# Optimization experiments

Measured on AMD Instinct MI355X. Metric: run time of the kernel, lower is better.

The kernel has to match this reference:

```python
import jax, jax.numpy as jnp
import numpy as np

HEADS = 8
HEIGHT = 64
WIDTH = 64
LN_EPS = 1e-5


def setup_inputs() -> dict:
    key = jax.random.key(0)
    k1, k2, k3, k4 = jax.random.split(key, 4)
    B, N, D = 8, 4096, 512
    return {
        "x1": jax.random.normal(k1, (B, N, D), jnp.float32),
        "x2": jax.random.normal(k2, (B, N, D), jnp.float32),
        "conv_w": jax.random.normal(k3, (2 * D, D), jnp.float32) * 0.02,
        "conv_b": jax.random.normal(k4, (2 * D,), jnp.float32) * 0.02,
        "ln_w": jnp.ones((2 * D,), jnp.float32),
        "ln_b": jnp.zeros((2 * D,), jnp.float32),
    }


def reference(x1, x2, conv_w, conv_b, ln_w, ln_b):
    B, N, D = x1.shape
    Dk = x2.shape[-1]
    hk = Dk // HEADS  # key channels per head
    hv = D // HEADS   # value channels per head
    # [B, H, hk, N] and [B, H, hv, N] (channel-first like torch transpose(1,2))
    kq = jnp.transpose(x2, (0, 2, 1)).reshape(B, HEADS, hk, N)
    v = jnp.transpose(x1, (0, 2, 1)).reshape(B, HEADS, hv, N)
    key = jax.nn.softmax(kq, axis=-1)   # softmax over tokens N
    query = jax.nn.softmax(kq, axis=2)  # softmax over head channels
    # linear attention: context [B,H,hk,hv], attended [B,H,hv,N]
    context = jnp.einsum("bhkn,bhvn->bhkv", key, v)
    attended = jnp.einsum("bhkv,bhkn->bhvn", context, query)
    agg = attended.reshape(B, D, N)  # concat heads along channel dim
    # 1x1 conv D -> 2D, then permute to [B, N, 2D]
    y = jnp.einsum("ed,bdn->bne", conv_w, agg) + conv_b
    # LayerNorm over last dim
    mu = jnp.mean(y, axis=-1, keepdims=True)
    var = jnp.mean(jnp.square(y - mu), axis=-1, keepdims=True)
    return (y - mu) * jax.lax.rsqrt(var + LN_EPS) * ln_w + ln_b
```

## Files before the change

kernel.cpp:

```cpp
#include <hip/hip_runtime.h>
#include <hip/hip_bf16.h>


typedef short short8 __attribute__((ext_vector_type(8)));
typedef float f32x4 __attribute__((ext_vector_type(4)));
typedef unsigned int uint;
typedef unsigned short ushort;

__device__ __forceinline__ ushort f2bf(float x) {
  union { float f; uint u; } v; v.f = x;
  uint r = v.u + 0x7FFFu + ((v.u >> 16) & 1u);
  return (ushort)(r >> 16);
}

__device__ __forceinline__ void gld_lds16(const void* g, void* l) {
  __builtin_amdgcn_global_load_lds(
      (const __attribute__((address_space(1))) unsigned int*)g,
      (__attribute__((address_space(3))) unsigned int*)l, 16, 0, 0);
}

__global__ __launch_bounds__(512) void k1_colstats(const float* __restrict__ x2,
                                                   float* __restrict__ pmax,
                                                   float* __restrict__ psum) {
  int blk = blockIdx.x;
  int b = blk >> 5, ch = blk & 31;
  int d = threadIdx.x;
  const float* base = x2 + ((size_t)(b * 4096 + ch * 128) * 512) + d;
  float m = -1e30f, s = 0.f;
  for (int nn = 0; nn < 128; ++nn) {
    float v = base[(size_t)nn * 512];
    if (v > m) { s = s * __expf(m - v) + 1.f; m = v; }
    else       { s += __expf(v - m); }
  }
  int o = (b * 32 + ch) * 512 + d;
  pmax[o] = m; psum[o] = s;
}

__global__ __launch_bounds__(256) void k1b_combine(const float* __restrict__ pmax,
                                                   const float* __restrict__ psum,
                                                   float* __restrict__ M,
                                                   float* __restrict__ Z) {
  int gid = blockIdx.x * 256 + threadIdx.x;
  int b = gid >> 9, d = gid & 511;
  float m = -1e30f;
  for (int ch = 0; ch < 32; ++ch) m = fmaxf(m, pmax[(b * 32 + ch) * 512 + d]);
  float z = 0.f;
  for (int ch = 0; ch < 32; ++ch)
    z += psum[(b * 32 + ch) * 512 + d] * __expf(pmax[(b * 32 + ch) * 512 + d] - m);
  M[gid] = m; Z[gid] = z;
}

__global__ __launch_bounds__(256) void kzero(float* __restrict__ p) {
  p[blockIdx.x * 256 + threadIdx.x] = 0.f;
}

__global__ __launch_bounds__(256) void kwb(const float* __restrict__ w,
                                           ushort* __restrict__ wb) {
  int i = blockIdx.x * 256 + threadIdx.x;
  wb[i] = f2bf(w[i]);
}

__global__ __launch_bounds__(256) void k2_context(const float* __restrict__ x1,
                                                  const float* __restrict__ x2,
                                                  const float* __restrict__ M,
                                                  const float* __restrict__ Z,
                                                  float* __restrict__ ctx) {
  int blk = blockIdx.x;
  int s = blk & 15, h = (blk >> 4) & 7, b = blk >> 7;
  __shared__ alignas(16) ushort Esm[64 * 72];
  __shared__ alignas(16) ushort Vsm[64 * 72];
  int tid = threadIdx.x;
  int l = tid & 63, w = tid >> 6;
  int lr = l & 15, lg = l >> 4;
  f32x4 acc[4] = {};

  for (int sub = 0; sub < 4; ++sub) {
    int n0 = s * 256 + sub * 64;
    __syncthreads();
    #pragma unroll
    for (int i = 0; i < 16; ++i) {
      int idx = tid + i * 256;
      int kk = idx & 63, nn = idx >> 6;
      size_t g = ((size_t)(b * 4096 + n0 + nn)) * 512 + h * 64 + kk;
      float e = __expf(x2[g] - M[b * 512 + h * 64 + kk]);
      Esm[kk * 72 + nn] = f2bf(e);
      Vsm[kk * 72 + nn] = f2bf(x1[g]);
    }
    __syncthreads();
    #pragma unroll
    for (int k2 = 0; k2 < 2; ++k2) {
      short8 a = *(const short8*)&Esm[(w * 16 + lr) * 72 + k2 * 32 + lg * 8];
      #pragma unroll
      for (int n = 0; n < 4; ++n) {
        short8 bb = *(const short8*)&Vsm[(n * 16 + lr) * 72 + k2 * 32 + lg * 8];
        acc[n] = __builtin_amdgcn_mfma_f32_16x16x32_bf16(a, bb, acc[n], 0, 0, 0);
      }
    }
  }
  #pragma unroll
  for (int n = 0; n < 4; ++n) {
    #pragma unroll
    for (int j = 0; j < 4; ++j) {
      int k = w * 16 + lg * 4 + j;
      int c = n * 16 + lr;
      float val = acc[n][j] / Z[b * 512 + h * 64 + k];
      atomicAdd(&ctx[((size_t)(b * 8 + h)) * 4096 + k * 64 + c], val);
    }
  }
}

__global__ __launch_bounds__(512) void k3_agg(const float* __restrict__ x2,
                                              const float* __restrict__ ctx,
                                              ushort* __restrict__ agg) {
  int blk = blockIdx.x;
  int b = blk >> 5, s2 = blk & 31;
  int tid = threadIdx.x;
  int w = tid >> 6;
  int l = tid & 63;
  float creg[64];
  #pragma unroll
  for (int k = 0; k < 64; ++k)
    creg[k] = ctx[((size_t)(b * 8 + w)) * 4096 + k * 64 + l];

  for (int tt = 0; tt < 128; ++tt) {
    int t = s2 * 128 + tt;
    float val = x2[((size_t)(b * 4096 + t)) * 512 + w * 64 + l];
    float m = val;
    #pragma unroll
    for (int o = 32; o > 0; o >>= 1) m = fmaxf(m, __shfl_xor(m, o));
    float e = __expf(val - m);
    float z = e;
    #pragma unroll
    for (int o = 32; o > 0; o >>= 1) z += __shfl_xor(z, o);
    float acc = 0.f;
    #pragma unroll
    for (int k = 0; k < 64; ++k) {
      float ek = __int_as_float(__builtin_amdgcn_readlane(__float_as_int(e), k));
      acc += ek * creg[k];
    }
    acc /= z;
    agg[((size_t)(b * 4096 + t)) * 512 + w * 64 + l] = f2bf(acc);
  }
}

__global__ __launch_bounds__(256) void k4_gemm(const ushort* __restrict__ agg,
                                               const ushort* __restrict__ wb,
                                               const float* __restrict__ conv_b,
                                               float* __restrict__ out) {
  int bm = blockIdx.x >> 3;
  int bn = blockIdx.x & 7;
  __shared__ alignas(16) ushort Asm[128 * 32];
  __shared__ alignas(16) ushort Bsm[128 * 32];
  int tid = threadIdx.x;
  int l = tid & 63, w = tid >> 6;
  int lr = l & 15, lg = l >> 4;
  int wr = (w >> 1) * 64, wc = (w & 1) * 64;
  f32x4 acc[4][4] = {};
  int rowA = bm * 128, rowB = bn * 128;
  int srow = tid >> 2;
  int skel = (tid & 3) * 8;

  for (int k0 = 0; k0 < 512; k0 += 32) {
    __syncthreads();
    #pragma unroll
    for (int c = 0; c < 2; ++c) {
      const ushort* ga = agg + (size_t)(rowA + c * 64 + srow) * 512 + k0 + skel;
      const ushort* gb = wb  + (size_t)(rowB + c * 64 + srow) * 512 + k0 + skel;
      gld_lds16(ga, (char*)Asm + c * 4096 + w * 1024);
      gld_lds16(gb, (char*)Bsm + c * 4096 + w * 1024);
    }
    __syncthreads();
    short8 a[4], bf[4];
    #pragma unroll
    for (int m = 0; m < 4; ++m)
      a[m] = *(const short8*)&Asm[(wr + m * 16 + lr) * 32 + lg * 8];
    #pragma unroll
    for (int n = 0; n < 4; ++n)
      bf[n] = *(const short8*)&Bsm[(wc + n * 16 + lr) * 32 + lg * 8];
    #pragma unroll
    for (int m = 0; m < 4; ++m)
      #pragma unroll
      for (int n = 0; n < 4; ++n)
        acc[m][n] = __builtin_amdgcn_mfma_f32_16x16x32_bf16(a[m], bf[n], acc[m][n], 0, 0, 0);
  }

  #pragma unroll
  for (int n = 0; n < 4; ++n) {
    int col = rowB + wc + n * 16 + lr;
    float bv = conv_b[col];
    #pragma unroll
    for (int m = 0; m < 4; ++m) {
      int row0 = rowA + wr + m * 16 + lg * 4;
      #pragma unroll
      for (int j = 0; j < 4; ++j)
        out[(size_t)(row0 + j) * 1024 + col] = acc[m][n][j] + bv;
    }
  }
}

__global__ __launch_bounds__(256) void k5_ln(float* __restrict__ out,
                                             const float* __restrict__ lnw,
                                             const float* __restrict__ lnb) {
  int t = blockIdx.x;
  int tid = threadIdx.x;
  float4 v = ((const float4*)(out + (size_t)t * 1024))[tid];
  float s  = v.x + v.y + v.z + v.w;
  float s2 = v.x * v.x + v.y * v.y + v.z * v.z + v.w * v.w;
  #pragma unroll
  for (int o = 32; o > 0; o >>= 1) { s += __shfl_xor(s, o); s2 += __shfl_xor(s2, o); }
  __shared__ float red[8];
  int w = tid >> 6, l = tid & 63;
  if (l == 0) { red[w] = s; red[4 + w] = s2; }
  __syncthreads();
  s  = red[0] + red[1] + red[2] + red[3];
  s2 = red[4] + red[5] + red[6] + red[7];
  float mean = s * (1.f / 1024.f);
  float var  = s2 * (1.f / 1024.f) - mean * mean;
  float rstd = rsqrtf(fmaxf(var, 0.f) + 1e-5f);
  float4 wv = ((const float4*)lnw)[tid];
  float4 bv = ((const float4*)lnb)[tid];
  float4 o;
  o.x = (v.x - mean) * rstd * wv.x + bv.x;
  o.y = (v.y - mean) * rstd * wv.y + bv.y;
  o.z = (v.z - mean) * rstd * wv.z + bv.z;
  o.w = (v.w - mean) * rstd * wv.w + bv.w;
  ((float4*)(out + (size_t)t * 1024))[tid] = o;
}

extern "C" void kernel_launch(void* const* d_in, const int* in_sizes, int n_in,
                              void* d_out, int out_size, void* d_ws, size_t ws_size,
                              hipStream_t stream) {
  const float* x1     = (const float*)d_in[0];
  const float* x2     = (const float*)d_in[1];
  const float* conv_w = (const float*)d_in[2];
  const float* conv_b = (const float*)d_in[3];
  const float* ln_w   = (const float*)d_in[4];
  const float* ln_b   = (const float*)d_in[5];
  float* out = (float*)d_out;

  float* ws   = (float*)d_ws;
  float* M    = ws;
  float* Z    = M + 4096;
  float* pmax = Z + 4096;
  float* psum = pmax + 131072;
  float* ctx  = psum + 131072;
  ushort* aggb = (ushort*)(ctx + 262144);
  ushort* wbb  = aggb + 16777216;

  k1_colstats<<<256, 512, 0, stream>>>(x2, pmax, psum);
  k1b_combine<<<16, 256, 0, stream>>>(pmax, psum, M, Z);
  kzero<<<1024, 256, 0, stream>>>(ctx);
  kwb<<<2048, 256, 0, stream>>>(conv_w, wbb);
  k2_context<<<1024, 256, 0, stream>>>(x1, x2, M, Z, ctx);
  k3_agg<<<256, 512, 0, stream>>>(x2, ctx, aggb);
  k4_gemm<<<2048, 256, 0, stream>>>(aggb, wbb, conv_b, out);
  k5_ln<<<32768, 256, 0, stream>>>(out, ln_w, ln_b);
}
```

Baseline: 550.7 us.

## Fold per-batch context into conv weights and feed query softmax to GEMM

The attended-value step is reassociated: the per-head context is multiplied into the 1x1 conv weight to form a per-batch weight W2[b] = W·ctx. The big GEMM then consumes the channel-softmaxed query directly. This removes the serial readlane-based aggregation kernel, which had low occupancy, and replaces it with a vectorized softmax kernel plus a small weight-folding kernel. The cost is that each batch now has its own bf16 weight matrix, which reduces weight reuse across batches in the GEMM and adds the precision risk of rounding the folded weights to bf16.

```diff
diff --git a/kernel.cpp b/kernel.cpp
--- a/kernel.cpp
+++ b/kernel.cpp
@@ -54,12 +54,6 @@
   p[blockIdx.x * 256 + threadIdx.x] = 0.f;
 }
 
-__global__ __launch_bounds__(256) void kwb(const float* __restrict__ w,
-                                           ushort* __restrict__ wb) {
-  int i = blockIdx.x * 256 + threadIdx.x;
-  wb[i] = f2bf(w[i]);
-}
-
 __global__ __launch_bounds__(256) void k2_context(const float* __restrict__ x1,
                                                   const float* __restrict__ x2,
                                                   const float* __restrict__ M,
@@ -109,46 +103,78 @@
   }
 }
 
-__global__ __launch_bounds__(512) void k3_agg(const float* __restrict__ x2,
-                                              const float* __restrict__ ctx,
-                                              ushort* __restrict__ agg) {
-  int blk = blockIdx.x;
-  int b = blk >> 5, s2 = blk & 31;
-  int tid = threadIdx.x;
-  int w = tid >> 6;
-  int l = tid & 63;
-  float creg[64];
-  #pragma unroll
-  for (int k = 0; k < 64; ++k)
-    creg[k] = ctx[((size_t)(b * 8 + w)) * 4096 + k * 64 + l];
-
-  for (int tt = 0; tt < 128; ++tt) {
-    int t = s2 * 128 + tt;
-    float val = x2[((size_t)(b * 4096 + t)) * 512 + w * 64 + l];
-    float m = val;
-    #pragma unroll
-    for (int o = 32; o > 0; o >>= 1) m = fmaxf(m, __shfl_xor(m, o));
-    float e = __expf(val - m);
-    float z = e;
-    #pragma unroll
-    for (int o = 32; o > 0; o >>= 1) z += __shfl_xor(z, o);
-    float acc = 0.f;
-    #pragma unroll
-    for (int k = 0; k < 64; ++k) {
-      float ek = __int_as_float(__builtin_amdgcn_readlane(__float_as_int(e), k));
-      acc += ek * creg[k];
-    }
-    acc /= z;
-    agg[((size_t)(b * 4096 + t)) * 512 + w * 64 + l] = f2bf(acc);
-  }
-}
-
-__global__ __launch_bounds__(256) void k4_gemm(const ushort* __restrict__ agg,
-                                               const ushort* __restrict__ wb,
+__global__ __launch_bounds__(256) void kq_softmax(const float* __restrict__ x2,
+                                                  ushort* __restrict__ Q) {
+  int tid = threadIdx.x;
+  int tok = blockIdx.x * 2 + (tid >> 7);
+  int c4 = (tid & 127) * 4;
+  float4 v = *(const float4*)(x2 + (size_t)tok * 512 + c4);
+  float m = fmaxf(fmaxf(v.x, v.y), fmaxf(v.z, v.w));
+  #pragma unroll
+  for (int o = 1; o < 16; o <<= 1) m = fmaxf(m, __shfl_xor(m, o));
+  float ex = __expf(v.x - m), ey = __expf(v.y - m);
+  float ez = __expf(v.z - m), ew = __expf(v.w - m);
+  float z = ex + ey + ez + ew;
+  #pragma unroll
+  for (int o = 1; o < 16; o <<= 1) z += __shfl_xor(z, o);
+  float rz = 1.f / z;
+  ushort4 q;
+  q.x = f2bf(ex * rz); q.y = f2bf(ey * rz);
+  q.z = f2bf(ez * rz); q.w = f2bf(ew * rz);
+  *(ushort4*)(Q + (size_t)tok * 512 + c4) = q;
+}
+
+__global__ __launch_bounds__(256) void kw2(const float* __restrict__ W,
+                                           const float* __restrict__ ctx,
+                                           ushort* __restrict__ W2) {
+  int blk = blockIdx.x;
+  int ec = blk & 7, h = (blk >> 3) & 7, b = blk >> 6;
+  __shared__ float Csm[64 * 68];
+  __shared__ float Wsm[128 * 68];
+  int tid = threadIdx.x;
+  const float* cp = ctx + ((size_t)(b * 8 + h)) * 4096;
+  #pragma unroll
+  for (int i = 0; i < 4; ++i) {
+    int idx = tid + i * 256, k = idx >> 4, cc = (idx & 15) * 4;
+    float4 cv = *(const float4*)(cp + k * 64 + cc);
+    *(float4*)(Csm + k * 68 + cc) = cv;
+  }
+  int e0 = ec * 128;
+  #pragma unroll
+  for (int i = 0; i < 8; ++i) {
+    int idx = tid + i * 256, r = idx >> 4, cc = (idx & 15) * 4;
+    float4 wv = *(const float4*)(W + (size_t)(e0 + r) * 512 + h * 64 + cc);
+    *(float4*)(Wsm + r * 68 + cc) = wv;
+  }
+  __syncthreads();
+  int r = tid >> 3;
+  int kg = (tid & 7) * 8;
+  for (int rs = 0; rs < 4; ++rs) {
+    int row = rs * 32 + r;
+    float acc[8] = {0.f, 0.f, 0.f, 0.f, 0.f, 0.f, 0.f, 0.f};
+    #pragma unroll
+    for (int cc = 0; cc < 64; cc += 4) {
+      float4 wv = *(const float4*)(Wsm + row * 68 + cc);
+      #pragma unroll
+      for (int k = 0; k < 8; ++k) {
+        float4 cv = *(const float4*)(Csm + (kg + k) * 68 + cc);
+        acc[k] += wv.x * cv.x + wv.y * cv.y + wv.z * cv.z + wv.w * cv.w;
+      }
+    }
+    ushort* op = W2 + ((size_t)b << 19) + (size_t)(e0 + row) * 512 + h * 64 + kg;
+    #pragma unroll
+    for (int k = 0; k < 8; ++k) op[k] = f2bf(acc[k]);
+  }
+}
+
+__global__ __launch_bounds__(256) void k4_gemm(const ushort* __restrict__ Q,
+                                               const ushort* __restrict__ W2,
                                                const float* __restrict__ conv_b,
                                                float* __restrict__ out) {
-  int bm = blockIdx.x >> 3;
-  int bn = blockIdx.x & 7;
+  int blk = blockIdx.x;
+  int b = blk >> 8;
+  int bm = (blk >> 3) & 31;
+  int bn = blk & 7;
   __shared__ alignas(16) ushort Asm[128 * 32];
   __shared__ alignas(16) ushort Bsm[128 * 32];
   int tid = threadIdx.x;
@@ -156,7 +182,9 @@
   int lr = l & 15, lg = l >> 4;
   int wr = (w >> 1) * 64, wc = (w & 1) * 64;
   f32x4 acc[4][4] = {};
-  int rowA = bm * 128, rowB = bn * 128;
+  int rowA = b * 4096 + bm * 128;
+  int rowB = bn * 128;
+  const ushort* Wb = W2 + ((size_t)b << 19);
   int srow = tid >> 2;
   int skel = (tid & 3) * 8;
 
@@ -164,8 +192,8 @@
     __syncthreads();
     #pragma unroll
     for (int c = 0; c < 2; ++c) {
-      const ushort* ga = agg + (size_t)(rowA + c * 64 + srow) * 512 + k0 + skel;
-      const ushort* gb = wb  + (size_t)(rowB + c * 64 + srow) * 512 + k0 + skel;
+      const ushort* ga = Q  + (size_t)(rowA + c * 64 + srow) * 512 + k0 + skel;
+      const ushort* gb = Wb + (size_t)(rowB + c * 64 + srow) * 512 + k0 + skel;
       gld_lds16(ga, (char*)Asm + c * 4096 + w * 1024);
       gld_lds16(gb, (char*)Bsm + c * 4096 + w * 1024);
     }
@@ -244,15 +272,15 @@
   float* pmax = Z + 4096;
   float* psum = pmax + 131072;
   float* ctx  = psum + 131072;
-  ushort* aggb = (ushort*)(ctx + 262144);
-  ushort* wbb  = aggb + 16777216;
+  ushort* Qb  = (ushort*)(ctx + 262144);
+  ushort* W2b = Qb + 16777216;
 
   k1_colstats<<<256, 512, 0, stream>>>(x2, pmax, psum);
   k1b_combine<<<16, 256, 0, stream>>>(pmax, psum, M, Z);
   kzero<<<1024, 256, 0, stream>>>(ctx);
-  kwb<<<2048, 256, 0, stream>>>(conv_w, wbb);
   k2_context<<<1024, 256, 0, stream>>>(x1, x2, M, Z, ctx);
-  k3_agg<<<256, 512, 0, stream>>>(x2, ctx, aggb);
-  k4_gemm<<<2048, 256, 0, stream>>>(aggb, wbb, conv_b, out);
+  kq_softmax<<<16384, 256, 0, stream>>>(x2, Qb);
+  kw2<<<512, 256, 0, stream>>>(conv_w, ctx, W2b);
+  k4_gemm<<<2048, 256, 0, stream>>>(Qb, W2b, conv_b, out);
   k5_ln<<<32768, 256, 0, stream>>>(out, ln_w, ln_b);
 }
```

After: 511.8 us. 7.1% less time.
